# Kernel tuning notes

Hardware: AMD Instinct MI355X
Metric: run time of the kernel (lower is better)

Reference implementation:

```python
import jax, jax.numpy as jnp
import numpy as np
from jax import lax

B = 16
IMG = 384
P = 16
C = 3
DIM = 256
DEPTH = 6
HEADS = 4
DH = 64
INNER = HEADS * DH  # 256
MLP = 512
NC = 21
HP = IMG // P       # 24
N = HP * HP         # 576
PD = C * P * P      # 768
K = 16
SCALE = DH ** -0.5
NEG = -1e9


def _ln(x, g, b):
    mu = x.mean(-1, keepdims=True)
    var = ((x - mu) ** 2).mean(-1, keepdims=True)
    return (x - mu) / jnp.sqrt(var + 1e-5) * g + b


def _conv(x, w, b):
    y = lax.conv_general_dilated(x, w, (1, 1), 'SAME',
                                 dimension_numbers=('NCHW', 'OIHW', 'NCHW'))
    return y + b[None, :, None, None]


def _up2(x):
    b, c, h, w = x.shape
    return jax.image.resize(x, (b, c, 2 * h, 2 * w), 'bilinear')


def _attn(x, g, bt, qkv_w, out_w, out_b, alpha):
    xn = _ln(x, g, bt)
    qkv = xn @ qkv_w                              # [B,N,3*INNER]
    q, k, v = jnp.split(qkv, 3, axis=-1)
    def heads(t):
        return t.reshape(B, N, HEADS, DH).transpose(0, 2, 1, 3)  # b h n d
    q, k, v = heads(q), heads(k), heads(v)
    dots = jnp.einsum('bhid,bhjd->bhij', q, k) * SCALE           # [B,H,N,N]
    vals, idx = lax.top_k(dots, K)                               # [B,H,N,K]
    bi = jnp.arange(B)[:, None, None, None]
    hi = jnp.arange(HEADS)[None, :, None, None]
    ni = jnp.arange(N)[None, None, :, None]
    sparse = jnp.full(dots.shape, NEG, dots.dtype).at[bi, hi, ni, idx].set(vals)
    sparse_attn = jax.nn.softmax(sparse, axis=-1)
    global_attn = jax.nn.softmax(dots, axis=-1)
    a = jnp.clip(alpha, 0.0, 1.0)
    attn = (1 - a) * sparse_attn + a * global_attn
    out = jnp.einsum('bhij,bhjd->bhid', attn, v)                 # [B,H,N,DH]
    out = out.transpose(0, 2, 1, 3).reshape(B, N, INNER)
    return out @ out_w + out_b


def _forward(img, patch_w, patch_b, pos_emb,
             ln1_g, ln1_b, qkv_w, out_w, out_b, alpha,
             ln2_g, ln2_b, ff_w1, ff_b1, ff_w2, ff_b2,
             lnf_g, lnf_b,
             conv1_w, conv1_b, conv2_w, conv2_b, conv3_w, conv3_b):
    # patchify: b c (h p1) (w p2) -> b (h w) (p1 p2 c)
    x = img.reshape(B, C, HP, P, HP, P).transpose(0, 2, 4, 3, 5, 1).reshape(B, N, PD)
    x = x @ patch_w + patch_b + pos_emb
    for i in range(DEPTH):
        x = x + _attn(x, ln1_g[i], ln1_b[i], qkv_w[i], out_w[i], out_b[i], alpha[i])
        h = _ln(x, ln2_g[i], ln2_b[i])
        h = jax.nn.gelu(h @ ff_w1[i] + ff_b1[i], approximate=False)
        x = x + h @ ff_w2[i] + ff_b2[i]
    x = _ln(x, lnf_g, lnf_b)
    x = x.transpose(0, 2, 1).reshape(B, DIM, HP, HP)             # b d h w
    x = jax.nn.relu(_conv(x, conv1_w, conv1_b))
    x = _up2(x)
    x = jax.nn.relu(_conv(x, conv2_w, conv2_b))
    x = _up2(x)
    x = _conv(x, conv3_w, conv3_b)
    return jax.image.resize(x, (B, NC, IMG, IMG), 'bilinear')


def setup_inputs() -> dict:
    key = jax.random.key(0)
    ks = jax.random.split(key, 16)
    s = 0.02
    d = {
        'img': jax.random.normal(ks[0], (B, C, IMG, IMG), jnp.float32),
        'patch_w': jax.random.normal(ks[1], (PD, DIM)) * s,
        'patch_b': jnp.zeros((DIM,)),
        'pos_emb': jax.random.normal(ks[2], (1, N, DIM)) * s,
        'ln1_g': jnp.ones((DEPTH, DIM)), 'ln1_b': jnp.zeros((DEPTH, DIM)),
        'qkv_w': jax.random.normal(ks[3], (DEPTH, DIM, 3 * INNER)) * s,
        'out_w': jax.random.normal(ks[4], (DEPTH, INNER, DIM)) * s,
        'out_b': jnp.zeros((DEPTH, DIM)),
        'alpha': jnp.full((DEPTH,), 0.2),
        'ln2_g': jnp.ones((DEPTH, DIM)), 'ln2_b': jnp.zeros((DEPTH, DIM)),
        'ff_w1': jax.random.normal(ks[5], (DEPTH, DIM, MLP)) * s,
        'ff_b1': jnp.zeros((DEPTH, MLP)),
        'ff_w2': jax.random.normal(ks[6], (DEPTH, MLP, DIM)) * s,
        'ff_b2': jnp.zeros((DEPTH, DIM)),
        'lnf_g': jnp.ones((DIM,)), 'lnf_b': jnp.zeros((DIM,)),
        'conv1_w': jax.random.normal(ks[7], (DIM // 2, DIM, 3, 3)) * s,
        'conv1_b': jnp.zeros((DIM // 2,)),
        'conv2_w': jax.random.normal(ks[8], (DIM // 4, DIM // 2, 3, 3)) * s,
        'conv2_b': jnp.zeros((DIM // 4,)),
        'conv3_w': jax.random.normal(ks[9], (NC, DIM // 4, 1, 1)) * s,
        'conv3_b': jnp.zeros((NC,)),
    }
    return d


def reference(img, patch_w, patch_b, pos_emb,
              ln1_g, ln1_b, qkv_w, out_w, out_b, alpha,
              ln2_g, ln2_b, ff_w1, ff_b1, ff_w2, ff_b2,
              lnf_g, lnf_b,
              conv1_w, conv1_b, conv2_w, conv2_b, conv3_w, conv3_b):
    return _forward(img, patch_w, patch_b, pos_emb,
                    ln1_g, ln1_b, qkv_w, out_w, out_b, alpha,
                    ln2_g, ln2_b, ff_w1, ff_b1, ff_w2, ff_b2,
                    lnf_g, lnf_b,
                    conv1_w, conv1_b, conv2_w, conv2_b, conv3_w, conv3_b)
```

## Files before the change

kernel.cpp:

```cpp
#include <hip/hip_runtime.h>
#include <cfloat>
#include <cmath>

constexpr int NB    = 16;
constexpr int IMGSZ = 384;
constexpr int PSZ   = 16;
constexpr int NCH   = 3;
constexpr int DMODEL= 256;
constexpr int DEPTH = 6;
constexpr int NHEAD = 4;
constexpr int DHEAD = 64;
constexpr int DQKV  = 768;
constexpr int QKS   = 512;
constexpr int DMLP  = 512;
constexpr int NCLS  = 21;
constexpr int HPATCH= 24;
constexpr int NTOK  = 576;
constexpr int NPD   = 768;
constexpr int TOPK  = 16;
constexpr int NROWS = NB * NTOK;
constexpr int OUT_TOTAL = NB * NCLS * IMGSZ * IMGSZ;

constexpr int RPB    = 16;
constexpr int NBLK   = NTOK / RPB;
constexpr int CHUNK  = 64;
constexpr int NCHUNK = NTOK / CHUNK;
constexpr int SCP    = 577;
constexpr int PPS    = 584;

typedef __attribute__((ext_vector_type(8))) short bf16x8;
typedef __attribute__((ext_vector_type(4))) float f32x4;

__device__ __forceinline__ unsigned short f2bf(float f) {
    unsigned u = __builtin_bit_cast(unsigned, f);
    unsigned r = (u + 0x7FFFu + ((u >> 16) & 1u)) >> 16;
    return (unsigned short)r;
}
__device__ __forceinline__ float bf2f(unsigned short h) {
    unsigned u = ((unsigned)h) << 16;
    return __builtin_bit_cast(float, u);
}

__global__ __launch_bounds__(256) void k_castT(const float* __restrict__ src,
                                               unsigned short* __restrict__ dst,
                                               int K, int N) {
    int t = blockIdx.x * 256 + threadIdx.x;
    if (t >= K * N) return;
    size_t base = (size_t)blockIdx.y * K * N;
    int n = t / K, k = t - n * K;
    dst[base + t] = f2bf(src[base + (size_t)k * N + n]);
}

template <int IC>
__global__ __launch_bounds__(256) void k_castConv(const float* __restrict__ src,
                                                  unsigned short* __restrict__ dst,
                                                  int OC) {
    int t = blockIdx.x * 256 + threadIdx.x;
    if (t >= OC * 9 * IC) return;
    int oc = t / (9 * IC);
    int r = t - oc * 9 * IC;
    int tap = r / IC, ic = r - tap * IC;
    dst[t] = f2bf(src[((size_t)(oc * IC + ic)) * 9 + tap]);
}

__global__ __launch_bounds__(256) void k_patchify(const float* __restrict__ img,
                                                  unsigned short* __restrict__ A) {
    int t = blockIdx.x * 256 + threadIdx.x;
    if (t >= NROWS * NPD) return;
    int r  = t / NPD, pd = t - r * NPD;
    int b  = r / NTOK, n = r - b * NTOK;
    int hy = n / HPATCH, hx = n - hy * HPATCH;
    int c  = pd % NCH;  int q = pd / NCH;
    int p2 = q % PSZ;   int p1 = q / PSZ;
    A[t] = f2bf(img[(((size_t)(b * NCH + c)) * IMGSZ + hy * PSZ + p1) * IMGSZ + hx * PSZ + p2]);
}

template <int BM, int BN, int EPI, int CIN>
__global__ __launch_bounds__(256) void k_mm(
    const unsigned short* __restrict__ Abf,
    const unsigned short* __restrict__ Wt,
    const float* __restrict__ bias,
    float* __restrict__ outf,
    unsigned short* __restrict__ outb,
    unsigned short* __restrict__ outb2,
    unsigned short* __restrict__ vth,
    unsigned short* __restrict__ vtl,
    int M, int Nn, int K, int H, int Wd, int gxd, int gyd)
{
    constexpr int MF = BM / 32;
    constexpr int NF = BN / 32;
    constexpr bool GATHER = (CIN > 0);
    constexpr int AREP = BM * 4 / 256;
    constexpr int BREP = BN * 4 / 256;
    __shared__ __align__(16) short As[4][BM][8];
    __shared__ __align__(16) short Bs[4][BN][8];
    const int tid = threadIdx.x;
    const int p = blockIdx.x;
    const int xr = p & 7, xq = p >> 3;
    const int bm = (xr * (gyd >> 3) + xq / gxd) * BM;
    const int bn = (xq % gxd) * BN;
    const int lane = tid & 63, wid = tid >> 6;
    const int wm = wid >> 1, wn = wid & 1;
    const int l15 = lane & 15, lg = lane >> 4;

    int pb_[AREP], py_[AREP], px_[AREP];
    if (GATHER) {
        #pragma unroll
        for (int rep = 0; rep < AREP; ++rep) {
            int idx = rep * 256 + tid;
            int m = idx >> 2;
            int pix = bm + m;
            px_[rep] = pix % Wd;
            int r = pix / Wd;
            py_[rep] = r % H;
            pb_[rep] = r / H;
        }
    }

    f32x4 acc[MF][NF];
    #pragma unroll
    for (int i = 0; i < MF; ++i)
        #pragma unroll
        for (int j = 0; j < NF; ++j)
            acc[i][j] = (f32x4){0.f, 0.f, 0.f, 0.f};

    for (int k0 = 0; k0 < K; k0 += 32) {
        #pragma unroll
        for (int rep = 0; rep < AREP; ++rep) {
            int idx = rep * 256 + tid;
            int m = idx >> 2, kg = idx & 3;
            if (!GATHER) {
                *(bf16x8*)As[kg][m] =
                    *(const bf16x8*)(Abf + (size_t)(bm + m) * K + k0 + kg * 8);
            } else {
                int k = k0 + kg * 8;
                int tap = k / CIN;
                int ic = k - tap * CIN;
                int dy = tap / 3 - 1, dx = tap % 3 - 1;
                int yy = py_[rep] + dy, xx = px_[rep] + dx;
                bf16x8 v = (bf16x8){0, 0, 0, 0, 0, 0, 0, 0};
                if ((unsigned)yy < (unsigned)H && (unsigned)xx < (unsigned)Wd)
                    v = *(const bf16x8*)(Abf +
                        ((size_t)((pb_[rep] * H + yy) * Wd + xx)) * CIN + ic);
                *(bf16x8*)As[kg][m] = v;
            }
        }
        #pragma unroll
        for (int rep = 0; rep < BREP; ++rep) {
            int idx = rep * 256 + tid;
            int n = idx >> 2, kg = idx & 3;
            *(bf16x8*)Bs[kg][n] =
                *(const bf16x8*)(Wt + (size_t)(bn + n) * K + k0 + kg * 8);
        }
        __syncthreads();
        bf16x8 af[MF], bfv[NF];
        #pragma unroll
        for (int i = 0; i < MF; ++i)
            af[i] = *(const bf16x8*)As[lg][wm * (BM / 2) + i * 16 + l15];
        #pragma unroll
        for (int j = 0; j < NF; ++j)
            bfv[j] = *(const bf16x8*)Bs[lg][wn * (BN / 2) + j * 16 + l15];
        #pragma unroll
        for (int i = 0; i < MF; ++i)
            #pragma unroll
            for (int j = 0; j < NF; ++j)
                acc[i][j] = __builtin_amdgcn_mfma_f32_16x16x32_bf16(
                    af[i], bfv[j], acc[i][j], 0, 0, 0);
        __syncthreads();
    }

    if constexpr (EPI == 8) {
        #pragma unroll
        for (int i = 0; i < MF; ++i) {
            const int row0 = bm + wm * (BM / 2) + i * 16 + lg * 4;
            #pragma unroll
            for (int j = 0; j < NF; ++j) {
                const int col = bn + wn * (BN / 2) + j * 16 + l15;
                if (col < 512) {
                    #pragma unroll
                    for (int r = 0; r < 4; ++r) {
                        float v = acc[i][j][r];
                        unsigned short hi = f2bf(v);
                        outb[(size_t)(row0 + r) * QKS + col] = hi;
                        outb2[(size_t)(row0 + r) * QKS + col] = f2bf(v - bf2f(hi));
                    }
                } else {
                    const int d = col - 512, hh = d >> 6, dd = d & 63;
                    const int bb = row0 / NTOK, n = row0 % NTOK;
                    unsigned long long ph = 0ull, pl = 0ull;
                    #pragma unroll
                    for (int r = 0; r < 4; ++r) {
                        float v = acc[i][j][r];
                        unsigned short hi = f2bf(v);
                        unsigned short lo = f2bf(v - bf2f(hi));
                        ph |= (unsigned long long)hi << (16 * r);
                        pl |= (unsigned long long)lo << (16 * r);
                    }
                    const size_t off = (size_t)((bb * NHEAD + hh) * DHEAD + dd) * NTOK + n;
                    *(unsigned long long*)(vth + off) = ph;
                    *(unsigned long long*)(vtl + off) = pl;
                }
            }
        }
    } else {
        #pragma unroll
        for (int i = 0; i < MF; ++i) {
            const int row0 = bm + wm * (BM / 2) + i * 16 + lg * 4;
            #pragma unroll
            for (int j = 0; j < NF; ++j) {
                const int col = bn + wn * (BN / 2) + j * 16 + l15;
                #pragma unroll
                for (int r = 0; r < 4; ++r) {
                    const int rr = row0 + r;
                    float v = acc[i][j][r] + bias[col];
                    if (EPI == 2) v = 0.5f * v * (1.0f + erff(v * 0.70710678118f));
                    if (EPI == 4) v = fmaxf(v, 0.f);
                    outb[(size_t)rr * Nn + col] = f2bf(v);
                }
            }
        }
    }
}

template <int RES>
__global__ __launch_bounds__(256) void k_gemm_ln(
    const unsigned short* __restrict__ Abf,
    const unsigned short* __restrict__ Wt,
    const float* __restrict__ bias,
    const float* __restrict__ extra,
    const float* __restrict__ lng,
    const float* __restrict__ lnb,
    float* __restrict__ x,
    unsigned short* __restrict__ xn,
    int K, int gyd)
{
    constexpr int BM = 32;
    __shared__ __align__(16) short As[4][BM][8];
    __shared__ __align__(16) short Bs[4][256][8];
    __shared__ float redS[BM][4];
    __shared__ float redQ[BM][4];
    const int tid = threadIdx.x;
    const int p = blockIdx.x;
    const int xr = p & 7, xq = p >> 3;
    const int bm = (xr * (gyd >> 3) + xq) * BM;
    const int lane = tid & 63, wn = tid >> 6;
    const int l15 = lane & 15, lg = lane >> 4;

    f32x4 acc[2][4];
    #pragma unroll
    for (int i = 0; i < 2; ++i)
        #pragma unroll
        for (int j = 0; j < 4; ++j)
            acc[i][j] = (f32x4){0.f, 0.f, 0.f, 0.f};

    for (int k0 = 0; k0 < K; k0 += 32) {
        if (tid < BM * 4) {
            int m = tid >> 2, kg = tid & 3;
            *(bf16x8*)As[kg][m] = *(const bf16x8*)(Abf + (size_t)(bm + m) * K + k0 + kg * 8);
        }
        #pragma unroll
        for (int rep = 0; rep < 4; ++rep) {
            int idx = rep * 256 + tid;
            int n = idx >> 2, kg = idx & 3;
            *(bf16x8*)Bs[kg][n] = *(const bf16x8*)(Wt + (size_t)n * K + k0 + kg * 8);
        }
        __syncthreads();
        bf16x8 af[2], bfv[4];
        #pragma unroll
        for (int i = 0; i < 2; ++i)
            af[i] = *(const bf16x8*)As[lg][i * 16 + l15];
        #pragma unroll
        for (int j = 0; j < 4; ++j)
            bfv[j] = *(const bf16x8*)Bs[lg][wn * 64 + j * 16 + l15];
        #pragma unroll
        for (int i = 0; i < 2; ++i)
            #pragma unroll
            for (int j = 0; j < 4; ++j)
                acc[i][j] = __builtin_amdgcn_mfma_f32_16x16x32_bf16(
                    af[i], bfv[j], acc[i][j], 0, 0, 0);
        __syncthreads();
    }

    #pragma unroll
    for (int i = 0; i < 2; ++i) {
        #pragma unroll
        for (int j = 0; j < 4; ++j) {
            const int col = wn * 64 + j * 16 + l15;
            #pragma unroll
            for (int r = 0; r < 4; ++r) {
                const int rr = bm + i * 16 + lg * 4 + r;
                float v = acc[i][j][r] + bias[col];
                if (RES) v += x[(size_t)rr * DMODEL + col];
                else     v += extra[(size_t)(rr % NTOK) * DMODEL + col];
                x[(size_t)rr * DMODEL + col] = v;
                acc[i][j][r] = v;
            }
        }
    }
    float s[2][4];
    #pragma unroll
    for (int i = 0; i < 2; ++i)
        #pragma unroll
        for (int r = 0; r < 4; ++r)
            s[i][r] = ((acc[i][0][r] + acc[i][1][r]) + acc[i][2][r]) + acc[i][3][r];
    #pragma unroll
    for (int off = 1; off < 16; off <<= 1)
        #pragma unroll
        for (int i = 0; i < 2; ++i)
            #pragma unroll
            for (int r = 0; r < 4; ++r)
                s[i][r] += __shfl_xor(s[i][r], off);
    if (l15 == 0)
        #pragma unroll
        for (int i = 0; i < 2; ++i)
            #pragma unroll
            for (int r = 0; r < 4; ++r)
                redS[i * 16 + lg * 4 + r][wn] = s[i][r];
    __syncthreads();
    float mu[2][4];
    #pragma unroll
    for (int i = 0; i < 2; ++i)
        #pragma unroll
        for (int r = 0; r < 4; ++r) {
            const float* q = redS[i * 16 + lg * 4 + r];
            mu[i][r] = (((q[0] + q[1]) + q[2]) + q[3]) * (1.0f / DMODEL);
        }
    float qq[2][4];
    #pragma unroll
    for (int i = 0; i < 2; ++i)
        #pragma unroll
        for (int r = 0; r < 4; ++r) {
            float d0 = acc[i][0][r] - mu[i][r], d1 = acc[i][1][r] - mu[i][r];
            float d2 = acc[i][2][r] - mu[i][r], d3 = acc[i][3][r] - mu[i][r];
            qq[i][r] = ((d0 * d0 + d1 * d1) + d2 * d2) + d3 * d3;
        }
    #pragma unroll
    for (int off = 1; off < 16; off <<= 1)
        #pragma unroll
        for (int i = 0; i < 2; ++i)
            #pragma unroll
            for (int r = 0; r < 4; ++r)
                qq[i][r] += __shfl_xor(qq[i][r], off);
    if (l15 == 0)
        #pragma unroll
        for (int i = 0; i < 2; ++i)
            #pragma unroll
            for (int r = 0; r < 4; ++r)
                redQ[i * 16 + lg * 4 + r][wn] = qq[i][r];
    __syncthreads();
    #pragma unroll
    for (int i = 0; i < 2; ++i) {
        #pragma unroll
        for (int r = 0; r < 4; ++r) {
            const float* q = redQ[i * 16 + lg * 4 + r];
            float var = (((q[0] + q[1]) + q[2]) + q[3]) * (1.0f / DMODEL);
            float rstd = rsqrtf(var + 1e-5f);
            const int rr = bm + i * 16 + lg * 4 + r;
            #pragma unroll
            for (int j = 0; j < 4; ++j) {
                const int col = wn * 64 + j * 16 + l15;
                float o = (acc[i][j][r] - mu[i][r]) * rstd * lng[col] + lnb[col];
                xn[(size_t)rr * DMODEL + col] = f2bf(o);
            }
        }
    }
}

struct KF { bf16x8 h0, h1, l0, l1; };
__device__ __forceinline__ KF ldkf(const unsigned short* __restrict__ hi,
                                   const unsigned short* __restrict__ lo,
                                   size_t off) {
    KF f;
    f.h0 = *(const bf16x8*)(hi + off);
    f.h1 = *(const bf16x8*)(hi + off + 32);
    f.l0 = *(const bf16x8*)(lo + off);
    f.l1 = *(const bf16x8*)(lo + off + 32);
    return f;
}

__global__ __launch_bounds__(512, 8) void k_attn(
    const unsigned short* __restrict__ qhi,
    const unsigned short* __restrict__ qlo,
    const unsigned short* __restrict__ vthi,
    const unsigned short* __restrict__ vtlo,
    const float* __restrict__ alpha_l,
    unsigned short* __restrict__ ao) {
    __shared__ __align__(16) unsigned char ub[2 * RPB * PPS * 2];
    float* scp = (float*)ub;
    short* php = (short*)ub;
    float* red = (float*)ub;

    const int tid = threadIdx.x;
    const int lane = tid & 63;
    const int w = tid >> 6;
    const int par = w >> 2;
    const int ct = w & 3;
    const int l15 = lane & 15, lg = lane >> 4;
    const int xr = blockIdx.x & 7, xq = blockIdx.x >> 3;
    const int g = xr + 8 * (xq / NBLK);
    const int b = g >> 2, h = g & 3;
    const int i0 = (xq % NBLK) * RPB;

    bf16x8 aqh0, aqh1, aql0, aql1;
    {
        const size_t qoff = (size_t)(b * NTOK + i0 + l15) * QKS + h * DHEAD + lg * 8;
        aqh0 = *(const bf16x8*)(qhi + qoff);
        aqh1 = *(const bf16x8*)(qhi + qoff + 32);
        aql0 = *(const bf16x8*)(qlo + qoff);
        aql1 = *(const bf16x8*)(qlo + qoff + 32);
    }

    const size_t kRow = (size_t)(b * NTOK + ct * 16 + l15) * QKS + DMODEL + h * DHEAD + lg * 8;
    for (int c = par; c < NCHUNK; c += 2) {
        KF kc = ldkf(qhi, qlo, kRow + (size_t)c * CHUNK * QKS);
        f32x4 sD = (f32x4){0.f, 0.f, 0.f, 0.f};
        sD = __builtin_amdgcn_mfma_f32_16x16x32_bf16(aqh0, kc.h0, sD, 0, 0, 0);
        sD = __builtin_amdgcn_mfma_f32_16x16x32_bf16(aqh0, kc.l0, sD, 0, 0, 0);
        sD = __builtin_amdgcn_mfma_f32_16x16x32_bf16(aql0, kc.h0, sD, 0, 0, 0);
        sD = __builtin_amdgcn_mfma_f32_16x16x32_bf16(aqh1, kc.h1, sD, 0, 0, 0);
        sD = __builtin_amdgcn_mfma_f32_16x16x32_bf16(aqh1, kc.l1, sD, 0, 0, 0);
        sD = __builtin_amdgcn_mfma_f32_16x16x32_bf16(aql1, kc.h1, sD, 0, 0, 0);
        const int col = c * CHUNK + ct * 16 + l15;
        #pragma unroll
        for (int r = 0; r < 4; ++r)
            scp[(lg * 4 + r) * SCP + col] = sD[r] * 0.125f;
    }
    __syncthreads();

    float o_[2][9];
    const int r0 = 2 * w;
    #pragma unroll
    for (int rr = 0; rr < 2; ++rr)
        #pragma unroll
        for (int t = 0; t < 9; ++t)
            o_[rr][t] = scp[(r0 + rr) * SCP + t * 64 + lane];
    __syncthreads();

    unsigned msk[2] = {0u, 0u};
    float M_[2];
    for (int k = 0; k < TOPK; ++k) {
        float lm[2];
        #pragma unroll
        for (int rr = 0; rr < 2; ++rr) {
            float m0 = -FLT_MAX;
            #pragma unroll
            for (int t = 0; t < 9; ++t) {
                float v = ((msk[rr] >> t) & 1u) ? -FLT_MAX : o_[rr][t];
                m0 = fmaxf(m0, v);
            }
            lm[rr] = m0;
        }
        #pragma unroll
        for (int off = 1; off < 64; off <<= 1) {
            #pragma unroll
            for (int rr = 0; rr < 2; ++rr)
                lm[rr] = fmaxf(lm[rr], __shfl_xor(lm[rr], off));
        }
        if (k == 0) {
            #pragma unroll
            for (int rr = 0; rr < 2; ++rr) M_[rr] = lm[rr];
        }
        #pragma unroll
        for (int rr = 0; rr < 2; ++rr) {
            int js = -1;
            #pragma unroll
            for (int t = 0; t < 9; ++t) {
                if (js < 0) {
                    unsigned long long bal =
                        __ballot((((msk[rr] >> t) & 1u) == 0u) && (o_[rr][t] == lm[rr]));
                    if (bal) js = t * 64 + (int)__builtin_ctzll(bal);
                }
            }
            if ((js & 63) == lane) msk[rr] |= 1u << (js >> 6);
        }
    }

    const float al = fminf(fmaxf(alpha_l[0], 0.f), 1.f);
    float gs[2], ss[2];
    #pragma unroll
    for (int rr = 0; rr < 2; ++rr) {
        float g_ = 0.f, s_ = 0.f;
        #pragma unroll
        for (int t = 0; t < 9; ++t) {
            float e = __expf(o_[rr][t] - M_[rr]);
            g_ += e;
            if ((msk[rr] >> t) & 1u) s_ += e;
        }
        gs[rr] = g_; ss[rr] = s_;
    }
    #pragma unroll
    for (int off = 1; off < 64; off <<= 1) {
        #pragma unroll
        for (int rr = 0; rr < 2; ++rr) {
            gs[rr] += __shfl_xor(gs[rr], off);
            ss[rr] += __shfl_xor(ss[rr], off);
        }
    }
    float ca[2], cs[2];
    #pragma unroll
    for (int rr = 0; rr < 2; ++rr) {
        ca[rr] = al / gs[rr];
        cs[rr] = (1.f - al) / ss[rr];
    }

    #pragma unroll
    for (int rr = 0; rr < 2; ++rr) {
        const int row = r0 + rr;
        #pragma unroll
        for (int t = 0; t < 9; ++t) {
            float e = __expf(o_[rr][t] - M_[rr]);
            float wv = e * (ca[rr] + (((msk[rr] >> t) & 1u) ? cs[rr] : 0.f));
            unsigned short hi = f2bf(wv);
            php[row * PPS + t * 64 + lane] = (short)hi;
            php[RPB * PPS + row * PPS + t * 64 + lane] = (short)f2bf(wv - bf2f(hi));
        }
    }
    __syncthreads();

    const size_t vRow = (size_t)((b * NHEAD + h) * DHEAD + ct * 16 + l15) * NTOK + lg * 8;
    f32x4 acc = (f32x4){0.f, 0.f, 0.f, 0.f};
    KF vc = ldkf(vthi, vtlo, vRow + (size_t)par * CHUNK);
    for (int c = par; c < NCHUNK; c += 2) {
        KF vn;
        if (c + 2 < NCHUNK)
            vn = ldkf(vthi, vtlo, vRow + (size_t)(c + 2) * CHUNK);
        const short* pr = php + l15 * PPS + c * 64 + lg * 8;
        bf16x8 ah0 = *(const bf16x8*)(pr);
        bf16x8 ah1 = *(const bf16x8*)(pr + 32);
        bf16x8 al0 = *(const bf16x8*)(pr + RPB * PPS);
        bf16x8 al1 = *(const bf16x8*)(pr + RPB * PPS + 32);
        acc = __builtin_amdgcn_mfma_f32_16x16x32_bf16(ah0, vc.h0, acc, 0, 0, 0);
        acc = __builtin_amdgcn_mfma_f32_16x16x32_bf16(ah0, vc.l0, acc, 0, 0, 0);
        acc = __builtin_amdgcn_mfma_f32_16x16x32_bf16(al0, vc.h0, acc, 0, 0, 0);
        acc = __builtin_amdgcn_mfma_f32_16x16x32_bf16(ah1, vc.h1, acc, 0, 0, 0);
        acc = __builtin_amdgcn_mfma_f32_16x16x32_bf16(ah1, vc.l1, acc, 0, 0, 0);
        acc = __builtin_amdgcn_mfma_f32_16x16x32_bf16(al1, vc.h1, acc, 0, 0, 0);
        if (c + 2 < NCHUNK) vc = vn;
    }
    __syncthreads();
    if (par == 1) {
        #pragma unroll
        for (int r = 0; r < 4; ++r)
            red[(ct * 16 + l15) * 17 + lg * 4 + r] = acc[r];
    }
    __syncthreads();
    if (par == 0) {
        const int qrow = i0 + lg * 4;
        const int dcol = h * DHEAD + ct * 16 + l15;
        #pragma unroll
        for (int r = 0; r < 4; ++r) {
            float v = acc[r] + red[(ct * 16 + l15) * 17 + lg * 4 + r];
            ao[(size_t)(b * NTOK + qrow + r) * DMODEL + dcol] = f2bf(v);
        }
    }
}

__device__ __forceinline__ void bilin_axis(float sF, int H, int& i0, int& i1, float& f) {
    float fl = floorf(sF);
    f = sF - fl;
    int lo = (int)fl;
    i0 = lo < 0 ? 0 : (lo > H - 1 ? H - 1 : lo);
    int hi = lo + 1;
    i1 = hi < 0 ? 0 : (hi > H - 1 ? H - 1 : hi);
}

__global__ __launch_bounds__(256) void k_up2n(const unsigned short* __restrict__ in,
                                              unsigned short* __restrict__ outp,
                                              int Hin, int C) {
    const int Ho = 2 * Hin;
    const int CG = C / 8;
    const int total = NB * Ho * Ho * CG;
    int t = blockIdx.x * 256 + threadIdx.x;
    if (t >= total) return;
    int cg = t % CG; int r = t / CG;
    int x = r % Ho; r /= Ho;
    int y = r % Ho; int b = r / Ho;
    int i0, i1, j0, j1; float fy, fx;
    bilin_axis(0.5f * y - 0.25f, Hin, i0, i1, fy);
    bilin_axis(0.5f * x - 0.25f, Hin, j0, j1, fx);
    const unsigned short* base = in + (size_t)b * Hin * Hin * C + cg * 8;
    const bf16x8 p00 = *(const bf16x8*)(base + (size_t)(i0 * Hin + j0) * C);
    const bf16x8 p01 = *(const bf16x8*)(base + (size_t)(i0 * Hin + j1) * C);
    const bf16x8 p10 = *(const bf16x8*)(base + (size_t)(i1 * Hin + j0) * C);
    const bf16x8 p11 = *(const bf16x8*)(base + (size_t)(i1 * Hin + j1) * C);
    bf16x8 o;
    #pragma unroll
    for (int e = 0; e < 8; ++e) {
        float v = (1.f - fy) * ((1.f - fx) * bf2f((unsigned short)p00[e]) + fx * bf2f((unsigned short)p01[e]))
                + fy        * ((1.f - fx) * bf2f((unsigned short)p10[e]) + fx * bf2f((unsigned short)p11[e]));
        o[e] = (short)f2bf(v);
    }
    *(bf16x8*)(outp + (size_t)t * 8) = o;
}

__global__ __launch_bounds__(256) void k_conv3n(const unsigned short* __restrict__ in,
                                                const float* __restrict__ w,
                                                const float* __restrict__ bias,
                                                float* __restrict__ outp) {
    __shared__ float ws_[NCLS * 64];
    for (int i = threadIdx.x; i < NCLS * 64; i += 256) ws_[i] = w[i];
    __syncthreads();
    int t = blockIdx.x * 256 + threadIdx.x;
    if (t >= NB * 9216) return;
    int pix = t % 9216, b = t / 9216;
    float xv[64];
    const unsigned short* p = in + (size_t)t * 64;
    #pragma unroll
    for (int c = 0; c < 8; ++c) {
        bf16x8 v = *(const bf16x8*)(p + c * 8);
        #pragma unroll
        for (int e = 0; e < 8; ++e) xv[c * 8 + e] = bf2f((unsigned short)v[e]);
    }
    float* op = outp + (size_t)b * NCLS * 9216 + pix;
    #pragma unroll
    for (int o = 0; o < NCLS; ++o) {
        float acc = bias[o];
        #pragma unroll
        for (int ic = 0; ic < 64; ++ic) acc += ws_[o * 64 + ic] * xv[ic];
        op[(size_t)o * 9216] = acc;
    }
}

__global__ __launch_bounds__(256) void k_resize4(const float* __restrict__ in,
                                                 float* __restrict__ outp) {
    int t = blockIdx.x * 256 + threadIdx.x;
    if (t >= OUT_TOTAL) return;
    int x = t % IMGSZ; int r = t / IMGSZ; int y = r % IMGSZ; int bc = r / IMGSZ;
    int i0, i1, j0, j1; float fy, fx;
    bilin_axis(0.25f * y - 0.375f, 96, i0, i1, fy);
    bilin_axis(0.25f * x - 0.375f, 96, j0, j1, fx);
    const float* p = in + (size_t)bc * 9216;
    outp[t] = (1.f - fy) * ((1.f - fx) * p[i0 * 96 + j0] + fx * p[i0 * 96 + j1])
            + fy        * ((1.f - fx) * p[i1 * 96 + j0] + fx * p[i1 * 96 + j1]);
}

extern "C" void kernel_launch(void* const* d_in, const int* in_sizes, int n_in,
                              void* d_out, int out_size, void* d_ws, size_t ws_size,
                              hipStream_t stream) {
    const float* img     = (const float*)d_in[0];
    const float* patch_w = (const float*)d_in[1];
    const float* patch_b = (const float*)d_in[2];
    const float* pos_emb = (const float*)d_in[3];
    const float* ln1_g   = (const float*)d_in[4];
    const float* ln1_b   = (const float*)d_in[5];
    const float* qkv_w   = (const float*)d_in[6];
    const float* out_w   = (const float*)d_in[7];
    const float* out_b   = (const float*)d_in[8];
    const float* alpha   = (const float*)d_in[9];
    const float* ln2_g   = (const float*)d_in[10];
    const float* ln2_b   = (const float*)d_in[11];
    const float* ff_w1   = (const float*)d_in[12];
    const float* ff_b1   = (const float*)d_in[13];
    const float* ff_w2   = (const float*)d_in[14];
    const float* ff_b2   = (const float*)d_in[15];
    const float* lnf_g   = (const float*)d_in[16];
    const float* lnf_b   = (const float*)d_in[17];
    const float* conv1_w = (const float*)d_in[18];
    const float* conv1_b = (const float*)d_in[19];
    const float* conv2_w = (const float*)d_in[20];
    const float* conv2_b = (const float*)d_in[21];
    const float* conv3_w = (const float*)d_in[22];
    const float* conv3_b = (const float*)d_in[23];

    float* x = (float*)d_ws;
    unsigned short* qkv_hi = (unsigned short*)(x + (size_t)NROWS * DMODEL);
    unsigned short* qkv_lo = qkv_hi + (size_t)NROWS * QKS;
    unsigned short* xn_bf  = qkv_lo + (size_t)NROWS * QKS;
    unsigned short* ao_bf  = xn_bf + (size_t)NROWS * DMODEL;
    unsigned short* h_bf   = ao_bf + (size_t)NROWS * DMODEL;
    unsigned short* pA     = h_bf + (size_t)NROWS * DMLP;
    unsigned short* wts    = pA + (size_t)NROWS * NPD;
    unsigned short* pwt  = wts;
    unsigned short* qwt  = pwt  + 768 * 256;
    unsigned short* owt  = qwt  + 6 * 768 * 256;
    unsigned short* f1wt = owt  + 6 * 256 * 256;
    unsigned short* f2wt = f1wt + 6 * 256 * 512;
    unsigned short* c1wt = f2wt + 6 * 512 * 256;
    unsigned short* c2wt = c1wt + 128 * 9 * 256;
    unsigned short* vthi = c2wt + 64 * 9 * 128;
    unsigned short* vtlo = vthi + (size_t)64 * 64 * NTOK;
    unsigned short* c1n = ao_bf;
    unsigned short* u1n = h_bf;
    unsigned short* c2n = xn_bf;
    unsigned short* u2n = qkv_hi;
    float* c3 = (float*)pA;

    k_castT<<<dim3(768, 1), 256, 0, stream>>>(patch_w, pwt, NPD, DMODEL);
    k_castT<<<dim3(768, 6), 256, 0, stream>>>(qkv_w, qwt, DMODEL, DQKV);
    k_castT<<<dim3(256, 6), 256, 0, stream>>>(out_w, owt, DMODEL, DMODEL);
    k_castT<<<dim3(512, 6), 256, 0, stream>>>(ff_w1, f1wt, DMODEL, DMLP);
    k_castT<<<dim3(512, 6), 256, 0, stream>>>(ff_w2, f2wt, DMLP, DMODEL);
    k_castConv<256><<<1152, 256, 0, stream>>>(conv1_w, c1wt, 128);
    k_castConv<128><<<288, 256, 0, stream>>>(conv2_w, c2wt, 64);

    k_patchify<<<(NROWS * NPD + 255) / 256, 256, 0, stream>>>(img, pA);
    k_gemm_ln<0><<<288, 256, 0, stream>>>(
        pA, pwt, patch_b, pos_emb, ln1_g, ln1_b, x, xn_bf, NPD, 288);

    for (int l = 0; l < DEPTH; ++l) {
        k_mm<128, 128, 8, 0><<<6 * 72, 256, 0, stream>>>(
            xn_bf, qwt + (size_t)l * DQKV * DMODEL, nullptr,
            nullptr, qkv_hi, qkv_lo, vthi, vtlo,
            NROWS, DQKV, DMODEL, 0, 0, 6, 72);
        k_attn<<<NBLK * NHEAD * NB, 512, 0, stream>>>(
            qkv_hi, qkv_lo, vthi, vtlo, alpha + l, ao_bf);
        k_gemm_ln<1><<<288, 256, 0, stream>>>(
            ao_bf, owt + (size_t)l * DMODEL * DMODEL, out_b + l * DMODEL, nullptr,
            ln2_g + l * DMODEL, ln2_b + l * DMODEL, x, xn_bf, DMODEL, 288);
        k_mm<128, 128, 2, 0><<<4 * 72, 256, 0, stream>>>(
            xn_bf, f1wt + (size_t)l * DMLP * DMODEL, ff_b1 + l * DMLP,
            nullptr, h_bf, nullptr, nullptr, nullptr,
            NROWS, DMLP, DMODEL, 0, 0, 4, 72);
        const float* ng = (l + 1 < DEPTH) ? (ln1_g + (l + 1) * DMODEL) : lnf_g;
        const float* nb = (l + 1 < DEPTH) ? (ln1_b + (l + 1) * DMODEL) : lnf_b;
        k_gemm_ln<1><<<288, 256, 0, stream>>>(
            h_bf, f2wt + (size_t)l * DMODEL * DMLP, ff_b2 + l * DMODEL, nullptr,
            ng, nb, x, xn_bf, DMLP, 288);
    }

    k_mm<64, 128, 4, 256><<<1 * 144, 256, 0, stream>>>(
        xn_bf, c1wt, conv1_b, nullptr, c1n, nullptr, nullptr, nullptr,
        NROWS, 128, 9 * 256, 24, 24, 1, 144);
    k_up2n<<<(NB * 48 * 48 * 16 + 255) / 256, 256, 0, stream>>>(c1n, u1n, 24, 128);
    k_mm<128, 64, 4, 128><<<1 * 288, 256, 0, stream>>>(
        u1n, c2wt, conv2_b, nullptr, c2n, nullptr, nullptr, nullptr,
        NB * 48 * 48, 64, 9 * 128, 48, 48, 1, 288);
    k_up2n<<<(NB * 96 * 96 * 8 + 255) / 256, 256, 0, stream>>>(c2n, u2n, 48, 64);
    k_conv3n<<<(NB * 9216 + 255) / 256, 256, 0, stream>>>(u2n, conv3_w, conv3_b, c3);
    k_resize4<<<(OUT_TOTAL + 255) / 256, 256, 0, stream>>>(c3, (float*)d_out);
}
```

Measured before the change: 1.293 ms.

## Merge weight casts, prefetch V earlier, vectorize resize, retile conv1 GEMM

Folds the five weight-cast launches into one kernel that picks its source and destination from blockIdx.y. In attention, the first V fragment load now starts before the softmax/top-k phase so its latency is hidden. The final 4x bilinear resize writes four outputs per thread with a float4 store and shares the row math across them. The conv1 GEMM tile narrows to 64 columns to double the block count. Together these aim to cut launch overhead, memory latency and store traffic. The early V load holds extra registers live across the top-k phase.

```diff
diff --git a/kernel.cpp b/kernel.cpp
--- a/kernel.cpp
+++ b/kernel.cpp
@@ -41,14 +41,28 @@
     return __builtin_bit_cast(float, u);
 }
 
-__global__ __launch_bounds__(256) void k_castT(const float* __restrict__ src,
-                                               unsigned short* __restrict__ dst,
-                                               int K, int N) {
+__global__ __launch_bounds__(256) void k_castAll(
+    const float* __restrict__ patch_w, const float* __restrict__ qkv_w,
+    const float* __restrict__ out_w,   const float* __restrict__ ff_w1,
+    const float* __restrict__ ff_w2,
+    unsigned short* __restrict__ pwt,  unsigned short* __restrict__ qwt,
+    unsigned short* __restrict__ owt,  unsigned short* __restrict__ f1wt,
+    unsigned short* __restrict__ f2wt) {
+    const int y = blockIdx.y;
+    const float* src; unsigned short* dst; int K, N;
+    if (y == 0)      { src = patch_w; dst = pwt; K = 768; N = 256; }
+    else if (y < 7)  { int l = y - 1;  K = 256; N = 768;
+                       src = qkv_w + (size_t)l * K * N; dst = qwt + (size_t)l * K * N; }
+    else if (y < 13) { int l = y - 7;  K = 256; N = 256;
+                       src = out_w + (size_t)l * K * N; dst = owt + (size_t)l * K * N; }
+    else if (y < 19) { int l = y - 13; K = 256; N = 512;
+                       src = ff_w1 + (size_t)l * K * N; dst = f1wt + (size_t)l * K * N; }
+    else             { int l = y - 19; K = 512; N = 256;
+                       src = ff_w2 + (size_t)l * K * N; dst = f2wt + (size_t)l * K * N; }
     int t = blockIdx.x * 256 + threadIdx.x;
     if (t >= K * N) return;
-    size_t base = (size_t)blockIdx.y * K * N;
     int n = t / K, k = t - n * K;
-    dst[base + t] = f2bf(src[base + (size_t)k * N + n]);
+    dst[t] = f2bf(src[(size_t)k * N + n]);
 }
 
 template <int IC>
@@ -425,6 +439,8 @@
         for (int r = 0; r < 4; ++r)
             scp[(lg * 4 + r) * SCP + col] = sD[r] * 0.125f;
     }
+    const size_t vRow = (size_t)((b * NHEAD + h) * DHEAD + ct * 16 + l15) * NTOK + lg * 8;
+    KF vc = ldkf(vthi, vtlo, vRow + (size_t)par * CHUNK);
     __syncthreads();
 
     float o_[2][9];
@@ -517,9 +533,7 @@
     }
     __syncthreads();
 
-    const size_t vRow = (size_t)((b * NHEAD + h) * DHEAD + ct * 16 + l15) * NTOK + lg * 8;
     f32x4 acc = (f32x4){0.f, 0.f, 0.f, 0.f};
-    KF vc = ldkf(vthi, vtlo, vRow + (size_t)par * CHUNK);
     for (int c = par; c < NCHUNK; c += 2) {
         KF vn;
         if (c + 2 < NCHUNK)
@@ -624,14 +638,27 @@
 __global__ __launch_bounds__(256) void k_resize4(const float* __restrict__ in,
                                                  float* __restrict__ outp) {
     int t = blockIdx.x * 256 + threadIdx.x;
-    if (t >= OUT_TOTAL) return;
-    int x = t % IMGSZ; int r = t / IMGSZ; int y = r % IMGSZ; int bc = r / IMGSZ;
-    int i0, i1, j0, j1; float fy, fx;
+    if (t >= OUT_TOTAL / 4) return;
+    const int xq = t % (IMGSZ / 4);
+    int r = t / (IMGSZ / 4);
+    const int y = r % IMGSZ;
+    const int bc = r / IMGSZ;
+    int i0, i1; float fy;
     bilin_axis(0.25f * y - 0.375f, 96, i0, i1, fy);
-    bilin_axis(0.25f * x - 0.375f, 96, j0, j1, fx);
     const float* p = in + (size_t)bc * 9216;
-    outp[t] = (1.f - fy) * ((1.f - fx) * p[i0 * 96 + j0] + fx * p[i0 * 96 + j1])
-            + fy        * ((1.f - fx) * p[i1 * 96 + j0] + fx * p[i1 * 96 + j1]);
+    const float* row0 = p + i0 * 96;
+    const float* row1 = p + i1 * 96;
+    float4 o;
+    float* oe = (float*)&o;
+    #pragma unroll
+    for (int e = 0; e < 4; ++e) {
+        const int x = xq * 4 + e;
+        int j0, j1; float fx;
+        bilin_axis(0.25f * x - 0.375f, 96, j0, j1, fx);
+        oe[e] = (1.f - fy) * ((1.f - fx) * row0[j0] + fx * row0[j1])
+              + fy        * ((1.f - fx) * row1[j0] + fx * row1[j1]);
+    }
+    *(float4*)(outp + (size_t)t * 4) = o;
 }
 
 extern "C" void kernel_launch(void* const* d_in, const int* in_sizes, int n_in,
@@ -685,11 +712,8 @@
     unsigned short* u2n = qkv_hi;
     float* c3 = (float*)pA;
 
-    k_castT<<<dim3(768, 1), 256, 0, stream>>>(patch_w, pwt, NPD, DMODEL);
-    k_castT<<<dim3(768, 6), 256, 0, stream>>>(qkv_w, qwt, DMODEL, DQKV);
-    k_castT<<<dim3(256, 6), 256, 0, stream>>>(out_w, owt, DMODEL, DMODEL);
-    k_castT<<<dim3(512, 6), 256, 0, stream>>>(ff_w1, f1wt, DMODEL, DMLP);
-    k_castT<<<dim3(512, 6), 256, 0, stream>>>(ff_w2, f2wt, DMLP, DMODEL);
+    k_castAll<<<dim3(768, 25), 256, 0, stream>>>(
+        patch_w, qkv_w, out_w, ff_w1, ff_w2, pwt, qwt, owt, f1wt, f2wt);
     k_castConv<256><<<1152, 256, 0, stream>>>(conv1_w, c1wt, 128);
     k_castConv<128><<<288, 256, 0, stream>>>(conv2_w, c2wt, 64);
 
@@ -718,14 +742,14 @@
             ng, nb, x, xn_bf, DMLP, 288);
     }
 
-    k_mm<64, 128, 4, 256><<<1 * 144, 256, 0, stream>>>(
+    k_mm<64, 64, 4, 256><<<2 * 144, 256, 0, stream>>>(
         xn_bf, c1wt, conv1_b, nullptr, c1n, nullptr, nullptr, nullptr,
-        NROWS, 128, 9 * 256, 24, 24, 1, 144);
+        NROWS, 128, 9 * 256, 24, 24, 2, 144);
     k_up2n<<<(NB * 48 * 48 * 16 + 255) / 256, 256, 0, stream>>>(c1n, u1n, 24, 128);
     k_mm<128, 64, 4, 128><<<1 * 288, 256, 0, stream>>>(
         u1n, c2wt, conv2_b, nullptr, c2n, nullptr, nullptr, nullptr,
         NB * 48 * 48, 64, 9 * 128, 48, 48, 1, 288);
     k_up2n<<<(NB * 96 * 96 * 8 + 255) / 256, 256, 0, stream>>>(c2n, u2n, 48, 64);
     k_conv3n<<<(NB * 9216 + 255) / 256, 256, 0, stream>>>(u2n, conv3_w, conv3_b, c3);
-    k_resize4<<<(OUT_TOTAL + 255) / 256, 256, 0, stream>>>(c3, (float*)d_out);
-}
+    k_resize4<<<(OUT_TOTAL / 4 + 255) / 256, 256, 0, stream>>>(c3, (float*)d_out);
+}
```

After: 1.281 ms. Within noise of the previous version (-0.9%).
